# Optimization experiments

Measured on AMD Instinct MI355X. Metric: run time of the kernel, lower is better.

The kernel has to match this reference:

```python
import jax, jax.numpy as jnp
import numpy as np

B, L, H, HD, NK, NQ = 2, 1024, 2048, 64, 4, 32
NPREV = NQ - NK  # 28 KV heads gathered from previous layers


def _rotate_half(x):
    x1, x2 = jnp.split(x, 2, axis=-1)
    return jnp.concatenate((-x2, x1), axis=-1)


def _apply_rope(cos, sin, x):
    length = x.shape[-2]
    return x * cos[..., -length:, :] + _rotate_half(x) * sin[..., -length:, :]


def setup_inputs() -> dict:
    key = jax.random.key(0)
    ks = jax.random.split(key, 7)
    hidden_states = jax.random.normal(ks[0], (B, L, H), jnp.float32)
    prev_k = jax.random.normal(ks[1], (B, NPREV, L, HD), jnp.float32)
    prev_v = jax.random.normal(ks[2], (B, NPREV, L, HD), jnp.float32)
    s = 0.02
    Wq = jax.random.normal(ks[3], (NQ * HD, H), jnp.float32) * s
    Wk = jax.random.normal(ks[4], (NK * HD, H), jnp.float32) * s
    Wv = jax.random.normal(ks[5], (NK * HD, H), jnp.float32) * s
    Wo = jax.random.normal(ks[6], (H, NQ * HD), jnp.float32) * s
    # RoPE tables (duplicated-half layout matching rotate_half)
    inv_freq = 1.0 / (10000.0 ** (jnp.arange(0, HD, 2, dtype=jnp.float32) / HD))
    freqs = jnp.arange(L, dtype=jnp.float32)[:, None] * inv_freq[None, :]
    emb = jnp.concatenate((freqs, freqs), axis=-1)  # [L, HD]
    cos = jnp.cos(emb)[None, None]  # [1,1,L,HD]
    sin = jnp.sin(emb)[None, None]
    attention_mask = jnp.tril(jnp.ones((L, L), dtype=bool))[None, None]  # [1,1,L,L]
    return {"hidden_states": hidden_states, "prev_k": prev_k, "prev_v": prev_v,
            "Wq": Wq, "Wk": Wk, "Wv": Wv, "Wo": Wo,
            "cos": cos, "sin": sin, "attention_mask": attention_mask}


def reference(hidden_states, prev_k, prev_v, Wq, Wk, Wv, Wo, cos, sin, attention_mask):
    Bv, Lv, _ = hidden_states.shape
    # QKV projections (torch Linear: x @ W.T)
    q = (hidden_states @ Wq.T).reshape(Bv, Lv, NQ, HD).transpose(0, 2, 1, 3)  # [B,NQ,L,HD]
    k_new = (hidden_states @ Wk.T).reshape(Bv, Lv, NK, HD).transpose(0, 2, 1, 3)
    v_new = (hidden_states @ Wv.T).reshape(Bv, Lv, NK, HD).transpose(0, 2, 1, 3)
    # DeCAN cross-layer cache update: stack previous layers' KV heads + current
    k = jnp.concatenate((prev_k, k_new), axis=1)  # [B,NQ,L,HD]
    v = jnp.concatenate((prev_v, v_new), axis=1)
    # RoPE after cache gather (same positions for all stacked layers)
    q = _apply_rope(cos, sin, q)
    k = _apply_rope(cos, sin, k)
    # SDPA with additive log-mask (log(bool) == 0 / -inf; broadcast == repeat)
    add_mask = jnp.where(attention_mask, jnp.float32(0.0), jnp.float32(-1e30))
    scores = jnp.einsum('bhqd,bhkd->bhqk', q, k) * (HD ** -0.5) + add_mask
    attn = jax.nn.softmax(scores, axis=-1)
    out = jnp.einsum('bhqk,bhkd->bhqd', attn, v)  # [B,NQ,L,HD]
    out = out.transpose(0, 2, 1, 3).reshape(Bv, Lv, NQ * HD)
    return out @ Wo.T  # [B,L,H]
```

## Files before the change

### kernel.cpp

```cpp
#include <hip/hip_runtime.h>
#include <stdint.h>

#define L_SEQ 1024
#define NHEAD 32
#define NPREV 28
#define HDIM  64
#define HID   2048
#define NPROJ 2560

typedef __bf16 bf16_t;
typedef bf16_t bf16x8 __attribute__((ext_vector_type(8)));
typedef float  f32x4  __attribute__((ext_vector_type(4)));

__device__ __forceinline__ ushort f2bf(float x) {
    union { float f; uint32_t u; } v; v.f = x;
    uint32_t r = v.u + 0x7fffu + ((v.u >> 16) & 1u);
    return (ushort)(r >> 16);
}
__device__ __forceinline__ ushort f2bf_t(float x) {
    union { float f; uint32_t u; } v; v.f = x;
    return (ushort)(v.u >> 16);
}
__device__ __forceinline__ float bf2f(ushort u) {
    union { uint32_t u; float f; } v; v.u = ((uint32_t)u) << 16; return v.f;
}
__device__ __forceinline__ void cvt8(float* dst, uint4 u) {
    union { uint32_t u; float f; } t;
    t.u = u.x << 16;         dst[0] = t.f;
    t.u = u.x & 0xffff0000u; dst[1] = t.f;
    t.u = u.y << 16;         dst[2] = t.f;
    t.u = u.y & 0xffff0000u; dst[3] = t.f;
    t.u = u.z << 16;         dst[4] = t.f;
    t.u = u.z & 0xffff0000u; dst[5] = t.f;
    t.u = u.w << 16;         dst[6] = t.f;
    t.u = u.w & 0xffff0000u; dst[7] = t.f;
}

#define GLB(p) ((const __attribute__((address_space(1))) void*)(p))
#define LDS(p) ((__attribute__((address_space(3))) void*)(p))

__global__ void cvt_all(const float* __restrict__ s0, const float* __restrict__ s1,
                        const float* __restrict__ s2, const float* __restrict__ s3,
                        const float* __restrict__ s4,
                        ushort* __restrict__ d0, ushort* __restrict__ d1,
                        ushort* __restrict__ d2, ushort* __restrict__ d3,
                        ushort* __restrict__ d4) {
    int blk = blockIdx.x;
    const float* src; ushort* dst; int idx;
    if      (blk < 4096) { src = s0; dst = d0; idx = blk; }
    else if (blk < 8192) { src = s1; dst = d1; idx = blk - 4096; }
    else if (blk < 8704) { src = s2; dst = d2; idx = blk - 8192; }
    else if (blk < 9216) { src = s3; dst = d3; idx = blk - 8704; }
    else                 { src = s4; dst = d4; idx = blk - 9216; }
    int i = idx * 256 + threadIdx.x;
    float4 v = ((const float4*)src)[i];
    ushort4 o;
    o.x = f2bf(v.x); o.y = f2bf(v.y); o.z = f2bf(v.z); o.w = f2bf(v.w);
    ((ushort4*)dst)[i] = o;
}

template <bool OUT_BF16>
__global__ __launch_bounds__(256, 3) void gemm_bt(const ushort* __restrict__ A,
                                                  const ushort* __restrict__ B,
                                                  void* __restrict__ C,
                                                  int M, int N, int K) {
    __shared__ __align__(16) ushort Ash[2 * 64 * 64];
    __shared__ __align__(16) ushort Bsh[2 * 128 * 64];
    const int tid  = threadIdx.x;
    const int lane = tid & 63;
    const int wave = tid >> 6;
    const int quad = lane >> 4;
    const int l16  = lane & 15;
    const int m0 = blockIdx.y * 64;
    const int n0 = blockIdx.x * 128;
    const int wm = (wave >> 1) * 32;
    const int wn = (wave & 1) * 64;

    f32x4 acc[2][4] = {};

    const int sb = ((tid & 3) ^ ((tid >> 3) & 3)) * 8;
    const ushort* Ag = A + (long)(m0 + (tid >> 2)) * K + sb;
    const ushort* Bg = B + (long)(n0 + (tid >> 2)) * K + sb;
    const int woff = wave * 512;
    const int swz = (quad ^ ((l16 >> 1) & 3)) * 8;

    __builtin_amdgcn_global_load_lds(GLB(Ag),                LDS(Ash + woff),               16, 0, 0);
    __builtin_amdgcn_global_load_lds(GLB(Ag + 32),           LDS(Ash + 2048 + woff),        16, 0, 0);
    __builtin_amdgcn_global_load_lds(GLB(Bg),                LDS(Bsh + woff),               16, 0, 0);
    __builtin_amdgcn_global_load_lds(GLB(Bg + 64L * K),      LDS(Bsh + 2048 + woff),        16, 0, 0);
    __builtin_amdgcn_global_load_lds(GLB(Bg + 32),           LDS(Bsh + 4096 + woff),        16, 0, 0);
    __builtin_amdgcn_global_load_lds(GLB(Bg + 64L * K + 32), LDS(Bsh + 4096 + 2048 + woff), 16, 0, 0);

    int cur = 0;
    for (int k0 = 0; k0 < K; k0 += 64) {
        __syncthreads();
        if (k0 + 64 < K) {
            const int na = (cur ^ 1) * 4096;
            const int nb = (cur ^ 1) * 8192;
            const ushort* Agn = Ag + k0 + 64;
            const ushort* Bgn = Bg + k0 + 64;
            __builtin_amdgcn_global_load_lds(GLB(Agn),                LDS(Ash + na + woff),               16, 0, 0);
            __builtin_amdgcn_global_load_lds(GLB(Agn + 32),           LDS(Ash + na + 2048 + woff),        16, 0, 0);
            __builtin_amdgcn_global_load_lds(GLB(Bgn),                LDS(Bsh + nb + woff),               16, 0, 0);
            __builtin_amdgcn_global_load_lds(GLB(Bgn + 64L * K),      LDS(Bsh + nb + 2048 + woff),        16, 0, 0);
            __builtin_amdgcn_global_load_lds(GLB(Bgn + 32),           LDS(Bsh + nb + 4096 + woff),        16, 0, 0);
            __builtin_amdgcn_global_load_lds(GLB(Bgn + 64L * K + 32), LDS(Bsh + nb + 4096 + 2048 + woff), 16, 0, 0);
        }
        const ushort* As = Ash + cur * 4096;
        const ushort* Bs = Bsh + cur * 8192;
#pragma unroll
        for (int h = 0; h < 2; h++) {
            bf16x8 af[2], bf[4];
#pragma unroll
            for (int i = 0; i < 2; i++)
                af[i] = *(const bf16x8*)(As + h * 2048 + (wm + i * 16 + l16) * 32 + swz);
#pragma unroll
            for (int i = 0; i < 4; i++)
                bf[i] = *(const bf16x8*)(Bs + h * 4096 + (wn + i * 16 + l16) * 32 + swz);
#pragma unroll
            for (int mi = 0; mi < 2; mi++)
#pragma unroll
                for (int ni = 0; ni < 4; ni++)
                    acc[mi][ni] = __builtin_amdgcn_mfma_f32_16x16x32_bf16(af[mi], bf[ni], acc[mi][ni], 0, 0, 0);
        }
        cur ^= 1;
    }
#pragma unroll
    for (int mi = 0; mi < 2; mi++)
#pragma unroll
        for (int ni = 0; ni < 4; ni++)
#pragma unroll
            for (int r = 0; r < 4; r++) {
                int m = m0 + wm + mi * 16 + quad * 4 + r;
                int n = n0 + wn + ni * 16 + l16;
                float v = acc[mi][ni][r];
                if (OUT_BF16) ((ushort*)C)[(long)m * N + n] = f2bf(v);
                else          ((float*)C)[(long)m * N + n]  = v;
            }
}

__global__ __launch_bounds__(256) void prep_qkv(const ushort* __restrict__ proj,
                                                const float* __restrict__ prev_k,
                                                const float* __restrict__ prev_v,
                                                const float* __restrict__ cosb,
                                                const float* __restrict__ sinb,
                                                ushort* __restrict__ Qr,
                                                ushort* __restrict__ Kr,
                                                ushort* __restrict__ Vt) {
    __shared__ __align__(16) ushort T[64 * 72];
    const int t  = threadIdx.x;
    const int l0 = blockIdx.x * 64;
    const int bh = blockIdx.y;
    const int b  = bh >> 5, h = bh & 31;
    const int r  = t >> 2;
    const int c0 = (t & 3) * 8;
    const int l  = l0 + r;
    const long prow = ((long)(b * L_SEQ + l)) * NPROJ;
    const long base = (long)bh * (L_SEQ * HDIM);

    float cv[8], sv[8];
    *(float4*)(cv)     = *(const float4*)(cosb + l * 64 + c0);
    *(float4*)(cv + 4) = *(const float4*)(cosb + l * 64 + c0 + 4);
    *(float4*)(sv)     = *(const float4*)(sinb + l * 64 + c0);
    *(float4*)(sv + 4) = *(const float4*)(sinb + l * 64 + c0 + 4);

    const float SC = 0.125f * 1.44269504f;

    {
        float xl[8], xh[8];
        cvt8(xl, *(const uint4*)(proj + prow + h * 64 + c0));
        cvt8(xh, *(const uint4*)(proj + prow + h * 64 + c0 + 32));
        ushort ol[8], oh[8];
#pragma unroll
        for (int i = 0; i < 8; i++) {
            ol[i] = f2bf((xl[i] * cv[i] - xh[i] * sv[i]) * SC);
            oh[i] = f2bf((xh[i] * cv[i] + xl[i] * sv[i]) * SC);
        }
        ushort* q = Qr + base + (long)l * 64;
        *(uint4*)(q + c0)      = *(uint4*)ol;
        *(uint4*)(q + c0 + 32) = *(uint4*)oh;
    }
    {
        float xl[8], xh[8];
        if (h < NPREV) {
            const float* pk = prev_k + (((long)b * NPREV + h) * L_SEQ + l) * 64;
            *(float4*)(xl)     = *(const float4*)(pk + c0);
            *(float4*)(xl + 4) = *(const float4*)(pk + c0 + 4);
            *(float4*)(xh)     = *(const float4*)(pk + c0 + 32);
            *(float4*)(xh + 4) = *(const float4*)(pk + c0 + 36);
        } else {
            cvt8(xl, *(const uint4*)(proj + prow + HID + (h - NPREV) * 64 + c0));
            cvt8(xh, *(const uint4*)(proj + prow + HID + (h - NPREV) * 64 + c0 + 32));
        }
        ushort ol[8], oh[8];
#pragma unroll
        for (int i = 0; i < 8; i++) {
            ol[i] = f2bf(xl[i] * cv[i] - xh[i] * sv[i]);
            oh[i] = f2bf(xh[i] * cv[i] + xl[i] * sv[i]);
        }
        ushort* k = Kr + base + (long)l * 64;
        *(uint4*)(k + c0)      = *(uint4*)ol;
        *(uint4*)(k + c0 + 32) = *(uint4*)oh;
    }
    {
        float xl[8], xh[8];
        if (h < NPREV) {
            const float* pv = prev_v + (((long)b * NPREV + h) * L_SEQ + l) * 64;
            *(float4*)(xl)     = *(const float4*)(pv + c0);
            *(float4*)(xl + 4) = *(const float4*)(pv + c0 + 4);
            *(float4*)(xh)     = *(const float4*)(pv + c0 + 32);
            *(float4*)(xh + 4) = *(const float4*)(pv + c0 + 36);
        } else {
            cvt8(xl, *(const uint4*)(proj + prow + HID + 256 + (h - NPREV) * 64 + c0));
            cvt8(xh, *(const uint4*)(proj + prow + HID + 256 + (h - NPREV) * 64 + c0 + 32));
        }
#pragma unroll
        for (int i = 0; i < 8; i++) {
            T[(c0 + i) * 72 + r]      = f2bf(xl[i]);
            T[(c0 + 32 + i) * 72 + r] = f2bf(xh[i]);
        }
    }
    __syncthreads();
    {
        const int lc = (t & 3) * 16;
        uint4 o0 = *(const uint4*)(T + r * 72 + lc);
        uint4 o1 = *(const uint4*)(T + r * 72 + lc + 8);
        ushort* og = Vt + base + (long)r * L_SEQ + l0 + lc;
        *(uint4*)og       = o0;
        *(uint4*)(og + 8) = o1;
    }
}

#define KP 68
__global__ __launch_bounds__(256, 4) void attn_mfma(const ushort* __restrict__ Qr,
                                                    const ushort* __restrict__ Kr,
                                                    const ushort* __restrict__ Vt,
                                                    ushort* __restrict__ Oa) {
    __shared__ __align__(16) ushort Ksh[64 * KP];
    __shared__ __align__(16) ushort Vsh[64 * KP];
    __shared__ __align__(16) ushort Psh[4][16 * KP];

    const int tid  = threadIdx.x;
    const int lane = tid & 63;
    const int wave = tid >> 6;
    const int quad = lane >> 4;
    const int l16  = lane & 15;
    const int bh   = blockIdx.y;
    const int q0   = (15 - (int)blockIdx.x) * 64;
    const long base = (long)bh * (L_SEQ * HDIM);

    bf16x8 qf0, qf1;
    {
        const ushort* qp = Qr + base + (long)(q0 + wave * 16 + l16) * HDIM + quad * 8;
        qf0 = *(const bf16x8*)qp;
        qf1 = *(const bf16x8*)(qp + 32);
    }
    float lr[4] = {};
    f32x4 o[4] = {};

    const int srow  = tid >> 2;
    const int scol  = (tid & 3) * 16;
    const int row_l = wave * 16 + quad * 4;

    uint4 ka, kb, va, vb;
    {
        const ushort* kg = Kr + base + (long)srow * HDIM + scol;
        ka = *(const uint4*)kg; kb = *(const uint4*)(kg + 8);
        const ushort* vg = Vt + base + (long)srow * L_SEQ + scol;
        va = *(const uint4*)vg; vb = *(const uint4*)(vg + 8);
    }

    for (int kv0 = 0; kv0 <= q0; kv0 += 64) {
        __syncthreads();
        *(uint4*)(Ksh + srow * KP + scol)     = ka;
        *(uint4*)(Ksh + srow * KP + scol + 8) = kb;
        *(uint4*)(Vsh + srow * KP + scol)     = va;
        *(uint4*)(Vsh + srow * KP + scol + 8) = vb;
        __syncthreads();
        if (kv0 + 64 <= q0) {
            const ushort* kg = Kr + base + (long)(kv0 + 64 + srow) * HDIM + scol;
            ka = *(const uint4*)kg; kb = *(const uint4*)(kg + 8);
            const ushort* vg = Vt + base + (long)srow * L_SEQ + kv0 + 64 + scol;
            va = *(const uint4*)vg; vb = *(const uint4*)(vg + 8);
        }

        f32x4 s[4] = {};
#pragma unroll
        for (int nt = 0; nt < 4; nt++) {
            bf16x8 kf0 = *(const bf16x8*)(Ksh + (nt * 16 + l16) * KP + quad * 8);
            bf16x8 kf1 = *(const bf16x8*)(Ksh + (nt * 16 + l16) * KP + 32 + quad * 8);
            s[nt] = __builtin_amdgcn_mfma_f32_16x16x32_bf16(qf0, kf0, s[nt], 0, 0, 0);
            s[nt] = __builtin_amdgcn_mfma_f32_16x16x32_bf16(qf1, kf1, s[nt], 0, 0, 0);
        }

        const bool diag = (kv0 == q0);
#pragma unroll
        for (int nt = 0; nt < 4; nt++) {
            const int col = nt * 16 + l16;
#pragma unroll
            for (int r = 0; r < 4; r++) {
                float p = __builtin_exp2f(s[nt][r]);
                if (diag && col > row_l + r) p = 0.f;
                lr[r] += p;
                Psh[wave][(quad * 4 + r) * KP + col] = f2bf_t(p);
            }
        }

#pragma unroll
        for (int ks = 0; ks < 2; ks++) {
            bf16x8 pf = *(const bf16x8*)(&Psh[wave][l16 * KP + ks * 32 + quad * 8]);
#pragma unroll
            for (int nt = 0; nt < 4; nt++) {
                bf16x8 vf = *(const bf16x8*)(Vsh + (nt * 16 + l16) * KP + ks * 32 + quad * 8);
                o[nt] = __builtin_amdgcn_mfma_f32_16x16x32_bf16(pf, vf, o[nt], 0, 0, 0);
            }
        }
    }

    const int b = bh >> 5, h = bh & 31;
#pragma unroll
    for (int r = 0; r < 4; r++) {
        float a = lr[r];
        a += __shfl_xor(a, 1); a += __shfl_xor(a, 2); a += __shfl_xor(a, 4); a += __shfl_xor(a, 8);
        float inv = 1.f / a;
        long orow = (long)(b * L_SEQ + q0 + wave * 16 + quad * 4 + r) * HID + h * 64;
#pragma unroll
        for (int nt = 0; nt < 4; nt++)
            Oa[orow + nt * 16 + l16] = f2bf(o[nt][r] * inv);
    }
}

extern "C" void kernel_launch(void* const* d_in, const int* in_sizes, int n_in,
                              void* d_out, int out_size, void* d_ws, size_t ws_size,
                              hipStream_t stream) {
    const float* hs     = (const float*)d_in[0];
    const float* prev_k = (const float*)d_in[1];
    const float* prev_v = (const float*)d_in[2];
    const float* Wq     = (const float*)d_in[3];
    const float* Wk     = (const float*)d_in[4];
    const float* Wv     = (const float*)d_in[5];
    const float* Wo     = (const float*)d_in[6];
    const float* cosb   = (const float*)d_in[7];
    const float* sinb   = (const float*)d_in[8];
    float* out = (float*)d_out;

    ushort* hs_bf   = (ushort*)d_ws;
    ushort* wqkv_bf = hs_bf + 2048L * 2048;
    ushort* wo_bf   = wqkv_bf + 2560L * 2048;
    ushort* proj    = wo_bf + 2048L * 2048;
    ushort* Qr      = proj + 2048L * 2560;
    ushort* Kr      = Qr + 4194304;
    ushort* Vt      = Kr + 4194304;
    ushort* Oa      = Vt + 4194304;

    cvt_all<<<13312, 256, 0, stream>>>(hs, Wq, Wk, Wv, Wo,
                                       hs_bf, wqkv_bf,
                                       wqkv_bf + 2048L * 2048,
                                       wqkv_bf + 2304L * 2048,
                                       wo_bf);
    gemm_bt<true><<<dim3(20, 32), 256, 0, stream>>>(hs_bf, wqkv_bf, proj, 2048, 2560, 2048);
    prep_qkv<<<dim3(16, 64), 256, 0, stream>>>(proj, prev_k, prev_v, cosb, sinb, Qr, Kr, Vt);
    attn_mfma<<<dim3(16, 64), 256, 0, stream>>>(Qr, Kr, Vt, Oa);
    gemm_bt<false><<<dim3(16, 32), 256, 0, stream>>>(Oa, wo_bf, out, 2048, 2048, 2048);
}
```

Measured before the change: 241.0 us.

## Split-K both GEMMs in two with bf16 partials and swap attention grid order

Both projection GEMMs now split the K dimension across blockIdx.z. This doubles the block count so the grid covers more of the machine. Each half writes bf16 partials: prep_qkv sums them for the QKV projection, and a new add2 kernel sums them for the output projection. The attention grid is transposed so heads vary fastest while heavy causal q-tiles are still issued first. In exchange there is extra partial-result traffic and one more launch, partials are rounded to bf16, and if the workspace is too small the code reuses the hidden_states input buffer as scratch.

```diff
diff --git a/kernel.cpp b/kernel.cpp
--- a/kernel.cpp
+++ b/kernel.cpp
@@ -59,13 +59,13 @@
     ((ushort4*)dst)[i] = o;
 }
 
-template <bool OUT_BF16>
 __global__ __launch_bounds__(256, 3) void gemm_bt(const ushort* __restrict__ A,
                                                   const ushort* __restrict__ B,
-                                                  void* __restrict__ C,
+                                                  ushort* __restrict__ C0,
+                                                  ushort* __restrict__ C1,
                                                   int M, int N, int K) {
-    __shared__ __align__(16) ushort Ash[2 * 64 * 64];
-    __shared__ __align__(16) ushort Bsh[2 * 128 * 64];
+    __shared__ __align__(16) ushort Ash[2 * 4096];
+    __shared__ __align__(16) ushort Bsh[2 * 8192];
     const int tid  = threadIdx.x;
     const int lane = tid & 63;
     const int wave = tid >> 6;
@@ -75,6 +75,9 @@
     const int n0 = blockIdx.x * 128;
     const int wm = (wave >> 1) * 32;
     const int wn = (wave & 1) * 64;
+    const int kb = blockIdx.z * (K >> 1);
+    const int ke = kb + (K >> 1);
+    ushort* C = blockIdx.z ? C1 : C0;
 
     f32x4 acc[2][4] = {};
 
@@ -84,17 +87,17 @@
     const int woff = wave * 512;
     const int swz = (quad ^ ((l16 >> 1) & 3)) * 8;
 
-    __builtin_amdgcn_global_load_lds(GLB(Ag),                LDS(Ash + woff),               16, 0, 0);
-    __builtin_amdgcn_global_load_lds(GLB(Ag + 32),           LDS(Ash + 2048 + woff),        16, 0, 0);
-    __builtin_amdgcn_global_load_lds(GLB(Bg),                LDS(Bsh + woff),               16, 0, 0);
-    __builtin_amdgcn_global_load_lds(GLB(Bg + 64L * K),      LDS(Bsh + 2048 + woff),        16, 0, 0);
-    __builtin_amdgcn_global_load_lds(GLB(Bg + 32),           LDS(Bsh + 4096 + woff),        16, 0, 0);
-    __builtin_amdgcn_global_load_lds(GLB(Bg + 64L * K + 32), LDS(Bsh + 4096 + 2048 + woff), 16, 0, 0);
+    __builtin_amdgcn_global_load_lds(GLB(Ag + kb),                LDS(Ash + woff),               16, 0, 0);
+    __builtin_amdgcn_global_load_lds(GLB(Ag + kb + 32),           LDS(Ash + 2048 + woff),        16, 0, 0);
+    __builtin_amdgcn_global_load_lds(GLB(Bg + kb),                LDS(Bsh + woff),               16, 0, 0);
+    __builtin_amdgcn_global_load_lds(GLB(Bg + 64L * K + kb),      LDS(Bsh + 2048 + woff),        16, 0, 0);
+    __builtin_amdgcn_global_load_lds(GLB(Bg + kb + 32),           LDS(Bsh + 4096 + woff),        16, 0, 0);
+    __builtin_amdgcn_global_load_lds(GLB(Bg + 64L * K + kb + 32), LDS(Bsh + 4096 + 2048 + woff), 16, 0, 0);
 
     int cur = 0;
-    for (int k0 = 0; k0 < K; k0 += 64) {
+    for (int k0 = kb; k0 < ke; k0 += 64) {
         __syncthreads();
-        if (k0 + 64 < K) {
+        if (k0 + 64 < ke) {
             const int na = (cur ^ 1) * 4096;
             const int nb = (cur ^ 1) * 8192;
             const ushort* Agn = Ag + k0 + 64;
@@ -133,13 +136,25 @@
             for (int r = 0; r < 4; r++) {
                 int m = m0 + wm + mi * 16 + quad * 4 + r;
                 int n = n0 + wn + ni * 16 + l16;
-                float v = acc[mi][ni][r];
-                if (OUT_BF16) ((ushort*)C)[(long)m * N + n] = f2bf(v);
-                else          ((float*)C)[(long)m * N + n]  = v;
+                C[(long)m * N + n] = f2bf(acc[mi][ni][r]);
             }
 }
 
-__global__ __launch_bounds__(256) void prep_qkv(const ushort* __restrict__ proj,
+__global__ void add2(const ushort* __restrict__ a, const ushort* __restrict__ b,
+                     float* __restrict__ out) {
+    int i = blockIdx.x * 256 + threadIdx.x;
+    uint4 ua = ((const uint4*)a)[i];
+    uint4 ub = ((const uint4*)b)[i];
+    float fa[8], fb[8];
+    cvt8(fa, ua); cvt8(fb, ub);
+    float4 o0 = {fa[0] + fb[0], fa[1] + fb[1], fa[2] + fb[2], fa[3] + fb[3]};
+    float4 o1 = {fa[4] + fb[4], fa[5] + fb[5], fa[6] + fb[6], fa[7] + fb[7]};
+    ((float4*)out)[2 * i]     = o0;
+    ((float4*)out)[2 * i + 1] = o1;
+}
+
+__global__ __launch_bounds__(256) void prep_qkv(const ushort* __restrict__ pa,
+                                                const ushort* __restrict__ pb,
                                                 const float* __restrict__ prev_k,
                                                 const float* __restrict__ prev_v,
                                                 const float* __restrict__ cosb,
@@ -167,14 +182,17 @@
     const float SC = 0.125f * 1.44269504f;
 
     {
-        float xl[8], xh[8];
-        cvt8(xl, *(const uint4*)(proj + prow + h * 64 + c0));
-        cvt8(xh, *(const uint4*)(proj + prow + h * 64 + c0 + 32));
+        float xl[8], xh[8], yl[8], yh[8];
+        cvt8(xl, *(const uint4*)(pa + prow + h * 64 + c0));
+        cvt8(xh, *(const uint4*)(pa + prow + h * 64 + c0 + 32));
+        cvt8(yl, *(const uint4*)(pb + prow + h * 64 + c0));
+        cvt8(yh, *(const uint4*)(pb + prow + h * 64 + c0 + 32));
         ushort ol[8], oh[8];
 #pragma unroll
         for (int i = 0; i < 8; i++) {
-            ol[i] = f2bf((xl[i] * cv[i] - xh[i] * sv[i]) * SC);
-            oh[i] = f2bf((xh[i] * cv[i] + xl[i] * sv[i]) * SC);
+            float a = xl[i] + yl[i], c = xh[i] + yh[i];
+            ol[i] = f2bf((a * cv[i] - c * sv[i]) * SC);
+            oh[i] = f2bf((c * cv[i] + a * sv[i]) * SC);
         }
         ushort* q = Qr + base + (long)l * 64;
         *(uint4*)(q + c0)      = *(uint4*)ol;
@@ -189,8 +207,13 @@
             *(float4*)(xh)     = *(const float4*)(pk + c0 + 32);
             *(float4*)(xh + 4) = *(const float4*)(pk + c0 + 36);
         } else {
-            cvt8(xl, *(const uint4*)(proj + prow + HID + (h - NPREV) * 64 + c0));
-            cvt8(xh, *(const uint4*)(proj + prow + HID + (h - NPREV) * 64 + c0 + 32));
+            float yl[8], yh[8];
+            cvt8(xl, *(const uint4*)(pa + prow + HID + (h - NPREV) * 64 + c0));
+            cvt8(xh, *(const uint4*)(pa + prow + HID + (h - NPREV) * 64 + c0 + 32));
+            cvt8(yl, *(const uint4*)(pb + prow + HID + (h - NPREV) * 64 + c0));
+            cvt8(yh, *(const uint4*)(pb + prow + HID + (h - NPREV) * 64 + c0 + 32));
+#pragma unroll
+            for (int i = 0; i < 8; i++) { xl[i] += yl[i]; xh[i] += yh[i]; }
         }
         ushort ol[8], oh[8];
 #pragma unroll
@@ -211,8 +234,13 @@
             *(float4*)(xh)     = *(const float4*)(pv + c0 + 32);
             *(float4*)(xh + 4) = *(const float4*)(pv + c0 + 36);
         } else {
-            cvt8(xl, *(const uint4*)(proj + prow + HID + 256 + (h - NPREV) * 64 + c0));
-            cvt8(xh, *(const uint4*)(proj + prow + HID + 256 + (h - NPREV) * 64 + c0 + 32));
+            float yl[8], yh[8];
+            cvt8(xl, *(const uint4*)(pa + prow + HID + 256 + (h - NPREV) * 64 + c0));
+            cvt8(xh, *(const uint4*)(pa + prow + HID + 256 + (h - NPREV) * 64 + c0 + 32));
+            cvt8(yl, *(const uint4*)(pb + prow + HID + 256 + (h - NPREV) * 64 + c0));
+            cvt8(yh, *(const uint4*)(pb + prow + HID + 256 + (h - NPREV) * 64 + c0 + 32));
+#pragma unroll
+            for (int i = 0; i < 8; i++) { xl[i] += yl[i]; xh[i] += yh[i]; }
         }
 #pragma unroll
         for (int i = 0; i < 8; i++) {
@@ -245,8 +273,8 @@
     const int wave = tid >> 6;
     const int quad = lane >> 4;
     const int l16  = lane & 15;
-    const int bh   = blockIdx.y;
-    const int q0   = (15 - (int)blockIdx.x) * 64;
+    const int bh   = blockIdx.x;
+    const int q0   = (15 - (int)blockIdx.y) * 64;
     const long base = (long)bh * (L_SEQ * HDIM);
 
     bf16x8 qf0, qf1;
@@ -353,13 +381,23 @@
     ushort* Vt      = Kr + 4194304;
     ushort* Oa      = Vt + 4194304;
 
+    ushort* proj_b;
+    if (ws_size >= (35651584UL + 5242880UL) * 2)
+        proj_b = Oa + 4194304;
+    else
+        proj_b = (ushort*)(void*)d_in[0];
+
+    ushort* outp_a = proj;
+    ushort* outp_b = Qr;
+
     cvt_all<<<13312, 256, 0, stream>>>(hs, Wq, Wk, Wv, Wo,
                                        hs_bf, wqkv_bf,
                                        wqkv_bf + 2048L * 2048,
                                        wqkv_bf + 2304L * 2048,
                                        wo_bf);
-    gemm_bt<true><<<dim3(20, 32), 256, 0, stream>>>(hs_bf, wqkv_bf, proj, 2048, 2560, 2048);
-    prep_qkv<<<dim3(16, 64), 256, 0, stream>>>(proj, prev_k, prev_v, cosb, sinb, Qr, Kr, Vt);
-    attn_mfma<<<dim3(16, 64), 256, 0, stream>>>(Qr, Kr, Vt, Oa);
-    gemm_bt<false><<<dim3(16, 32), 256, 0, stream>>>(Oa, wo_bf, out, 2048, 2048, 2048);
-}
+    gemm_bt<<<dim3(20, 32, 2), 256, 0, stream>>>(hs_bf, wqkv_bf, proj, proj_b, 2048, 2560, 2048);
+    prep_qkv<<<dim3(16, 64), 256, 0, stream>>>(proj, proj_b, prev_k, prev_v, cosb, sinb, Qr, Kr, Vt);
+    attn_mfma<<<dim3(64, 16), 256, 0, stream>>>(Qr, Kr, Vt, Oa);
+    gemm_bt<<<dim3(16, 32, 2), 256, 0, stream>>>(Oa, wo_bf, outp_a, outp_b, 2048, 2048, 2048);
+    add2<<<2048, 256, 0, stream>>>(outp_a, outp_b, out);
+}
```

Measured after the change: 237.5 us. No clear change (-1.4%).
